# Kernel optimization log

Measured on AMD Instinct MI355X. Metric: run time of the kernel, lower is better.

## Reference

```python
import jax, jax.numpy as jnp
import numpy as np

DIM = 96
K = 3
STRIDE = 1
PAD = 1
RED = 4
BN_EPS = 1e-5


def setup_inputs() -> dict:
    key = jax.random.key(0)
    ks = jax.random.split(key, 8)
    b, c, h, w = 32, DIM, 128, 128
    cr = DIM // RED
    return {
        "x": jax.random.normal(ks[0], (b, c, h, w), jnp.float32),
        "w1": jax.random.normal(ks[1], (cr, c), jnp.float32) * 0.1,          # conv1 1x1, no bias
        "gamma": jnp.ones((cr,), jnp.float32),
        "beta": jnp.zeros((cr,), jnp.float32),
        "running_mean": jax.random.normal(ks[2], (cr,), jnp.float32) * 0.1,
        "running_var": jax.random.uniform(ks[3], (cr,), jnp.float32, 0.5, 1.5),
        "w2": jax.random.normal(ks[4], (DIM * K * K, cr), jnp.float32) * 0.1,  # conv2 1x1
        "b2": jax.random.normal(ks[5], (DIM * K * K,), jnp.float32) * 0.1,
        "bias": jnp.zeros((DIM,), jnp.float32),
    }


def _dynamic_weight(x, w1, gamma, beta, running_mean, running_var, w2, b2):
    # AdaptiveAvgPool2d((1,1)) -> [b, c]
    pooled = jnp.mean(x, axis=(2, 3))
    # conv1 (1x1, no bias) on 1x1 spatial == matmul
    h1 = pooled @ w1.T  # [b, c//r]
    # BatchNorm2d in inference mode (running stats)
    h1 = (h1 - running_mean) * jax.lax.rsqrt(running_var + BN_EPS) * gamma + beta
    h1 = jax.nn.sigmoid(h1)
    # conv2 (1x1) == matmul + bias -> [b, dim*k*k]
    wdyn = h1 @ w2.T + b2
    return wdyn.reshape(x.shape[0], DIM, K, K)


def _per_sample_depthwise(x, weight, bias):
    # x: [b, c, h, w], weight: [b, c, k, k] -> per-sample depthwise conv
    def one(xi, wi):
        # xi: [c,h,w], wi: [c,k,k]
        out = jax.lax.conv_general_dilated(
            xi[None], wi[:, None],
            window_strides=(STRIDE, STRIDE),
            padding=[(PAD, PAD), (PAD, PAD)],
            dimension_numbers=("NCHW", "OIHW", "NCHW"),
            feature_group_count=DIM,
        )
        return out[0]

    y = jax.vmap(one)(x, weight)  # [b, c, h', w']
    return y + bias[None, :, None, None]


def reference(x, w1, gamma, beta, running_mean, running_var, w2, b2, bias):
    weight = _dynamic_weight(x, w1, gamma, beta, running_mean, running_var, w2, b2)
    return _per_sample_depthwise(x, weight, bias)
```

## Files before the change

kernel.cpp:

```cpp
#include <hip/hip_runtime.h>
#include <math.h>

#define C_DIM 96
#define CR 24
#define H_DIM 128
#define W_DIM 128
#define B_DIM 32
#define CHUNKS 4
#define ROWS_PER_CHUNK (H_DIM / CHUNKS)

typedef float nfloat4 __attribute__((ext_vector_type(4)));

__global__ void pool_kernel(const float* __restrict__ x, float* __restrict__ pooled) {
    int plane = blockIdx.x;
    const float4* xp = (const float4*)(x + (size_t)plane * (H_DIM * W_DIM));
    float s = 0.f;
    for (int i = threadIdx.x; i < 4096; i += 256) {
        float4 v = xp[i];
        s += v.x + v.y + v.z + v.w;
    }
    for (int off = 32; off; off >>= 1) s += __shfl_down(s, off, 64);
    __shared__ float ls[4];
    int lane = threadIdx.x & 63, wv = threadIdx.x >> 6;
    if (lane == 0) ls[wv] = s;
    __syncthreads();
    if (threadIdx.x == 0) {
        float t = ls[0] + ls[1] + ls[2] + ls[3];
        pooled[plane] = t * (1.f / (H_DIM * W_DIM));
    }
}

__global__ void __launch_bounds__(256) fused_dwconv_kernel(const float* __restrict__ x,
                                                           const float* __restrict__ pooled,
                                                           const float* __restrict__ w1,
                                                           const float* __restrict__ gamma,
                                                           const float* __restrict__ beta,
                                                           const float* __restrict__ rmean,
                                                           const float* __restrict__ rvar,
                                                           const float* __restrict__ w2,
                                                           const float* __restrict__ b2,
                                                           const float* __restrict__ bias,
                                                           float* __restrict__ out) {
    int tid = threadIdx.x;
    int plane0 = blockIdx.x * 2;
    int b = plane0 / C_DIM;
    int c0 = plane0 % C_DIM;

    __shared__ float pl[C_DIM];
    __shared__ float h1[CR];
    __shared__ float wsm[2][10];

    if (tid < C_DIM) pl[tid] = pooled[b * C_DIM + tid];
    __syncthreads();
    if (tid < CR) {
        float s = 0.f;
        const float* wr = w1 + tid * C_DIM;
        #pragma unroll 8
        for (int c = 0; c < C_DIM; c++) s += pl[c] * wr[c];
        s = (s - rmean[tid]) * rsqrtf(rvar[tid] + 1e-5f) * gamma[tid] + beta[tid];
        h1[tid] = 1.f / (1.f + expf(-s));
    }
    __syncthreads();
    if (tid < 20) {
        if (tid < 18) {
            int p = tid / 9, k = tid % 9;
            int row = (c0 + p) * 9 + k;
            float s = b2[row];
            const float* wr = w2 + row * CR;
            #pragma unroll
            for (int j = 0; j < CR; j++) s += h1[j] * wr[j];
            wsm[p][k] = s;
        } else {
            wsm[tid - 18][9] = bias[c0 + (tid - 18)];
        }
    }
    __syncthreads();

    int g = tid & 31;
    int chunk = (tid >> 5) & 3;
    int p = tid >> 7;
    int plane = plane0 + p;
    int col = g << 2;
    int r0 = chunk * ROWS_PER_CHUNK;

    const float* xp = x + (size_t)plane * (H_DIM * W_DIM);
    float* op = out + (size_t)plane * (H_DIM * W_DIM);
    const float* wv = wsm[p];
    float w00 = wv[0], w01 = wv[1], w02 = wv[2];
    float w10 = wv[3], w11 = wv[4], w12 = wv[5];
    float w20 = wv[6], w21 = wv[7], w22 = wv[8];
    float bb = wv[9];
    const bool leftEdge = (g == 0), rightEdge = (g == 31);

    float4 pv, cv, nv;
    float plh, prh, clh, crh, nlh, nrh;

    {
        int r = r0 - 1;
        float4 v;
        if (r >= 0) v = *(const float4*)(xp + r * W_DIM + col);
        else { v.x = v.y = v.z = v.w = 0.f; }
        float l = __shfl_up(v.w, 1, 64);
        float rr = __shfl_down(v.x, 1, 64);
        pv = v; plh = leftEdge ? 0.f : l; prh = rightEdge ? 0.f : rr;
    }
    {
        float4 v = *(const float4*)(xp + r0 * W_DIM + col);
        float l = __shfl_up(v.w, 1, 64);
        float rr = __shfl_down(v.x, 1, 64);
        cv = v; clh = leftEdge ? 0.f : l; crh = rightEdge ? 0.f : rr;
    }

    #pragma unroll 4
    for (int i = 0; i < ROWS_PER_CHUNK; i++) {
        int r = r0 + i;
        float4 v;
        if (r + 1 < H_DIM) v = *(const float4*)(xp + (r + 1) * W_DIM + col);
        else { v.x = v.y = v.z = v.w = 0.f; }
        float l = __shfl_up(v.w, 1, 64);
        float rr = __shfl_down(v.x, 1, 64);
        nv = v; nlh = leftEdge ? 0.f : l; nrh = rightEdge ? 0.f : rr;

        nfloat4 o;
        o.x = w00 * plh  + w01 * pv.x + w02 * pv.y
            + w10 * clh  + w11 * cv.x + w12 * cv.y
            + w20 * nlh  + w21 * nv.x + w22 * nv.y + bb;
        o.y = w00 * pv.x + w01 * pv.y + w02 * pv.z
            + w10 * cv.x + w11 * cv.y + w12 * cv.z
            + w20 * nv.x + w21 * nv.y + w22 * nv.z + bb;
        o.z = w00 * pv.y + w01 * pv.z + w02 * pv.w
            + w10 * cv.y + w11 * cv.z + w12 * cv.w
            + w20 * nv.y + w21 * nv.z + w22 * nv.w + bb;
        o.w = w00 * pv.z + w01 * pv.w + w02 * prh
            + w10 * cv.z + w11 * cv.w + w12 * crh
            + w20 * nv.z + w21 * nv.w + w22 * nrh + bb;
        __builtin_nontemporal_store(o, (nfloat4*)(op + r * W_DIM + col));

        pv = cv; plh = clh; prh = crh;
        cv = nv; clh = nlh; crh = nrh;
    }
}

extern "C" void kernel_launch(void* const* d_in, const int* in_sizes, int n_in,
                              void* d_out, int out_size, void* d_ws, size_t ws_size,
                              hipStream_t stream) {
    const float* x     = (const float*)d_in[0];
    const float* w1    = (const float*)d_in[1];
    const float* gamma = (const float*)d_in[2];
    const float* beta  = (const float*)d_in[3];
    const float* rmean = (const float*)d_in[4];
    const float* rvar  = (const float*)d_in[5];
    const float* w2    = (const float*)d_in[6];
    const float* b2    = (const float*)d_in[7];
    const float* bias  = (const float*)d_in[8];
    float* out = (float*)d_out;

    float* pooled = (float*)d_ws;

    pool_kernel<<<B_DIM * C_DIM, 256, 0, stream>>>(x, pooled);
    fused_dwconv_kernel<<<B_DIM * C_DIM / 2, 256, 0, stream>>>(
        x, pooled, w1, gamma, beta, rmean, rvar, w2, b2, bias, out);
}
```

Baseline: 386.7 us.

## Merge pooling and depthwise conv into one cooperative persistent kernel with reverse order

Replaces the two launches with one persistent cooperative kernel. Each block pools its plane pairs, waits at a grid-wide sync, then runs the dynamic weight and depthwise conv over the same pairs in reverse order, so the most recently read planes may still be in cache. This aims to cut launch overhead and some re-reading of x from HBM, at the cost of a grid barrier and fewer resident blocks. The grid size comes from an occupancy query capped at 768 blocks, and the code falls back to the two-kernel path if the cooperative launch fails.

Result: slower. 471.0 us (+21.8%).

```diff
diff --git a/kernel.cpp b/kernel.cpp
--- a/kernel.cpp
+++ b/kernel.cpp
@@ -1,5 +1,8 @@
 #include <hip/hip_runtime.h>
+#include <hip/hip_cooperative_groups.h>
 #include <math.h>
+
+namespace cg = cooperative_groups;
 
 #define C_DIM 96
 #define CR 24
@@ -8,8 +11,151 @@
 #define B_DIM 32
 #define CHUNKS 4
 #define ROWS_PER_CHUNK (H_DIM / CHUNKS)
+#define N_PLANES (B_DIM * C_DIM)
+#define N_PAIRS  (N_PLANES / 2)
+#define NBLK 768
 
 typedef float nfloat4 __attribute__((ext_vector_type(4)));
+
+__global__ void __launch_bounds__(256) merged_kernel(const float* __restrict__ x,
+                                                     float* __restrict__ pooled,
+                                                     const float* __restrict__ w1,
+                                                     const float* __restrict__ gamma,
+                                                     const float* __restrict__ beta,
+                                                     const float* __restrict__ rmean,
+                                                     const float* __restrict__ rvar,
+                                                     const float* __restrict__ w2,
+                                                     const float* __restrict__ b2,
+                                                     const float* __restrict__ bias,
+                                                     float* __restrict__ out) {
+    const int tid = threadIdx.x;
+    const int nb = gridDim.x;
+    const int kmax = (N_PAIRS - 1 - (int)blockIdx.x) / nb;
+
+    __shared__ float ls[4];
+    __shared__ float pl[C_DIM];
+    __shared__ float h1[CR];
+    __shared__ float wsm[2][10];
+
+    for (int k = 0; k <= kmax; ++k) {
+        int pair = blockIdx.x + k * nb;
+        #pragma unroll
+        for (int pp = 0; pp < 2; ++pp) {
+            int plane = pair * 2 + pp;
+            const float4* xp = (const float4*)(x + (size_t)plane * (H_DIM * W_DIM));
+            float s = 0.f;
+            for (int i = tid; i < 4096; i += 256) {
+                float4 v = xp[i];
+                s += v.x + v.y + v.z + v.w;
+            }
+            for (int off = 32; off; off >>= 1) s += __shfl_down(s, off, 64);
+            if ((tid & 63) == 0) ls[tid >> 6] = s;
+            __syncthreads();
+            if (tid == 0) pooled[plane] = (ls[0] + ls[1] + ls[2] + ls[3]) * (1.f / (H_DIM * W_DIM));
+            __syncthreads();
+        }
+    }
+
+    cg::this_grid().sync();
+
+    for (int k = kmax; k >= 0; --k) {
+        int pair = blockIdx.x + k * nb;
+        int plane0 = pair * 2;
+        int b = plane0 / C_DIM;
+        int c0 = plane0 % C_DIM;
+
+        if (tid < C_DIM) pl[tid] = pooled[b * C_DIM + tid];
+        __syncthreads();
+        if (tid < CR) {
+            float s = 0.f;
+            const float* wr = w1 + tid * C_DIM;
+            #pragma unroll 8
+            for (int c = 0; c < C_DIM; c++) s += pl[c] * wr[c];
+            s = (s - rmean[tid]) * rsqrtf(rvar[tid] + 1e-5f) * gamma[tid] + beta[tid];
+            h1[tid] = 1.f / (1.f + expf(-s));
+        }
+        __syncthreads();
+        if (tid < 20) {
+            if (tid < 18) {
+                int p = tid / 9, kk = tid % 9;
+                int row = (c0 + p) * 9 + kk;
+                float s = b2[row];
+                const float* wr = w2 + row * CR;
+                #pragma unroll
+                for (int j = 0; j < CR; j++) s += h1[j] * wr[j];
+                wsm[p][kk] = s;
+            } else {
+                wsm[tid - 18][9] = bias[c0 + (tid - 18)];
+            }
+        }
+        __syncthreads();
+
+        int g = tid & 31;
+        int chunk = (tid >> 5) & 3;
+        int p = tid >> 7;
+        int plane = plane0 + p;
+        int col = g << 2;
+        int r0 = chunk * ROWS_PER_CHUNK;
+
+        const float* xp = x + (size_t)plane * (H_DIM * W_DIM);
+        float* op = out + (size_t)plane * (H_DIM * W_DIM);
+        const float* wv = wsm[p];
+        float w00 = wv[0], w01 = wv[1], w02 = wv[2];
+        float w10 = wv[3], w11 = wv[4], w12 = wv[5];
+        float w20 = wv[6], w21 = wv[7], w22 = wv[8];
+        float bb = wv[9];
+        const bool leftEdge = (g == 0), rightEdge = (g == 31);
+
+        float4 pv, cv, nv;
+        float plh, prh, clh, crh, nlh, nrh;
+
+        {
+            int r = r0 - 1;
+            float4 v;
+            if (r >= 0) v = *(const float4*)(xp + r * W_DIM + col);
+            else { v.x = v.y = v.z = v.w = 0.f; }
+            float l = __shfl_up(v.w, 1, 64);
+            float rr = __shfl_down(v.x, 1, 64);
+            pv = v; plh = leftEdge ? 0.f : l; prh = rightEdge ? 0.f : rr;
+        }
+        {
+            float4 v = *(const float4*)(xp + r0 * W_DIM + col);
+            float l = __shfl_up(v.w, 1, 64);
+            float rr = __shfl_down(v.x, 1, 64);
+            cv = v; clh = leftEdge ? 0.f : l; crh = rightEdge ? 0.f : rr;
+        }
+
+        #pragma unroll 4
+        for (int i = 0; i < ROWS_PER_CHUNK; i++) {
+            int r = r0 + i;
+            float4 v;
+            if (r + 1 < H_DIM) v = *(const float4*)(xp + (r + 1) * W_DIM + col);
+            else { v.x = v.y = v.z = v.w = 0.f; }
+            float l = __shfl_up(v.w, 1, 64);
+            float rr = __shfl_down(v.x, 1, 64);
+            nv = v; nlh = leftEdge ? 0.f : l; nrh = rightEdge ? 0.f : rr;
+
+            nfloat4 o;
+            o.x = w00 * plh  + w01 * pv.x + w02 * pv.y
+                + w10 * clh  + w11 * cv.x + w12 * cv.y
+                + w20 * nlh  + w21 * nv.x + w22 * nv.y + bb;
+            o.y = w00 * pv.x + w01 * pv.y + w02 * pv.z
+                + w10 * cv.x + w11 * cv.y + w12 * cv.z
+                + w20 * nv.x + w21 * nv.y + w22 * nv.z + bb;
+            o.z = w00 * pv.y + w01 * pv.z + w02 * pv.w
+                + w10 * cv.y + w11 * cv.z + w12 * cv.w
+                + w20 * nv.y + w21 * nv.z + w22 * nv.w + bb;
+            o.w = w00 * pv.z + w01 * pv.w + w02 * prh
+                + w10 * cv.z + w11 * cv.w + w12 * crh
+                + w20 * nv.z + w21 * nv.w + w22 * nrh + bb;
+            __builtin_nontemporal_store(o, (nfloat4*)(op + r * W_DIM + col));
+
+            pv = cv; plh = clh; prh = crh;
+            cv = nv; clh = nlh; crh = nrh;
+        }
+        __syncthreads();
+    }
+}
 
 __global__ void pool_kernel(const float* __restrict__ x, float* __restrict__ pooled) {
     int plane = blockIdx.x;
@@ -157,7 +303,25 @@
 
     float* pooled = (float*)d_ws;
 
-    pool_kernel<<<B_DIM * C_DIM, 256, 0, stream>>>(x, pooled);
-    fused_dwconv_kernel<<<B_DIM * C_DIM / 2, 256, 0, stream>>>(
-        x, pooled, w1, gamma, beta, rmean, rvar, w2, b2, bias, out);
+    static int nb = 0;
+    if (nb == 0) {
+        int mb = 0;
+        hipError_t qe = hipOccupancyMaxActiveBlocksPerMultiprocessor(&mb, merged_kernel, 256, 0);
+        if (qe != hipSuccess || mb <= 0) { mb = 3; (void)hipGetLastError(); }
+        long cap = (long)mb * 256;
+        nb = (int)(cap < NBLK ? cap : NBLK);
+        if (nb < 1) nb = 1;
+    }
+
+    void* kargs[] = { (void*)&x, (void*)&pooled, (void*)&w1, (void*)&gamma, (void*)&beta,
+                      (void*)&rmean, (void*)&rvar, (void*)&w2, (void*)&b2, (void*)&bias,
+                      (void*)&out };
+    hipError_t e = hipLaunchCooperativeKernel((const void*)merged_kernel,
+                                              dim3(nb), dim3(256), kargs, 0, stream);
+    if (e != hipSuccess) {
+        (void)hipGetLastError();
+        pool_kernel<<<N_PLANES, 256, 0, stream>>>(x, pooled);
+        fused_dwconv_kernel<<<N_PAIRS, 256, 0, stream>>>(
+            x, pooled, w1, gamma, beta, rmean, rvar, w2, b2, bias, out);
+    }
 }
```
